# Optimization experiments

Hardware: AMD Instinct MI355X
Metric: run time of the kernel (lower is better)

Reference implementation:

```python
import jax, jax.numpy as jnp
import numpy as np

B, H, W, C = 64, 224, 224, 3
K = 16          # num_clusters
ITERS = 10      # num_iterations
N = H * W       # pixels per image


def _kmeans_single(x, key):
    # x: [N, D] pixels of one image
    # random shuffle -> first K rows as initial centroids (matches tf.random.shuffle + slice)
    perm = jax.random.permutation(key, N)
    cent0 = x[perm[:K]]  # [K, D]

    def step(cent, _):
        # pairwise squared distances: [K, N]
        d = jnp.sum(jnp.square(x[None, :, :] - cent[:, None, :]), axis=2)
        assign = jnp.argmin(d, axis=0)                      # [N] int
        onehot = jax.nn.one_hot(assign, K, dtype=x.dtype)   # [N, K]
        sums = onehot.T @ x                                 # [K, D]
        counts = jnp.sum(onehot, axis=0)[:, None]           # [K, 1]
        # mean of assigned pixels; empty cluster -> 0/0 = NaN, same as tf.reduce_mean of empty
        new_cent = sums / counts
        return new_cent, None

    cent, _ = jax.lax.scan(step, cent0, None, length=ITERS)
    return cent.reshape(K * C)  # tf.reshape(centroids, [dims*num_clusters]) on [K,D]


def setup_inputs() -> dict:
    key = jax.random.key(0)
    inputs = jax.random.uniform(key, (B, H, W, C), dtype=jnp.float32) * 255.0
    return {"inputs": inputs}


def reference(inputs):
    x = inputs.astype(jnp.float32).reshape(B, N, C)
    keys = jax.random.split(jax.random.key(42), B)
    return jax.vmap(_kmeans_single)(x, keys)  # [B, K*C]
```

## Files before the change

kernel.cpp:

```cpp
#include <hip/hip_runtime.h>
#include <stdint.h>


#define NB    64
#define NPIX  50176
#define NK    16
#define NCH   3
#define NITER 10
#define HBINS 2048
#define CANDCAP 1024
#define COLLCAP 128
#define NBLK  512
#define NGRP  8
#define GRPSZ (NBLK / NGRP)
#define CHUNK (NPIX / 8)
#define NQUADS (CHUNK / 4)

typedef unsigned long long u64;

struct KeyPair { uint32_t a, b; };

__device__ __forceinline__ uint32_t rotl32(uint32_t v, uint32_t r) {
  return (v << r) | (v >> (32u - r));
}
__device__ __forceinline__ void tf_round(uint32_t& x0, uint32_t& x1, uint32_t r) {
  x0 += x1; x1 = rotl32(x1, r); x1 ^= x0;
}

__device__ __forceinline__ KeyPair threefry(uint32_t k0, uint32_t k1,
                                            uint32_t x0, uint32_t x1) {
  const uint32_t ks2 = k0 ^ k1 ^ 0x1BD11BDAu;
  x0 += k0; x1 += k1;
  tf_round(x0, x1, 13u); tf_round(x0, x1, 15u); tf_round(x0, x1, 26u); tf_round(x0, x1, 6u);
  x0 += k1;  x1 += ks2 + 1u;
  tf_round(x0, x1, 17u); tf_round(x0, x1, 29u); tf_round(x0, x1, 16u); tf_round(x0, x1, 24u);
  x0 += ks2; x1 += k0 + 2u;
  tf_round(x0, x1, 13u); tf_round(x0, x1, 15u); tf_round(x0, x1, 26u); tf_round(x0, x1, 6u);
  x0 += k0;  x1 += k1 + 3u;
  tf_round(x0, x1, 17u); tf_round(x0, x1, 29u); tf_round(x0, x1, 16u); tf_round(x0, x1, 24u);
  x0 += k1;  x1 += ks2 + 4u;
  tf_round(x0, x1, 13u); tf_round(x0, x1, 15u); tf_round(x0, x1, 26u); tf_round(x0, x1, 6u);
  x0 += ks2; x1 += k0 + 5u;
  KeyPair r; r.a = x0; r.b = x1; return r;
}

__device__ __forceinline__ uint32_t sortkey(KeyPair S, uint32_t i) {
  KeyPair r = threefry(S.a, S.b, 0u, i);
  return r.a ^ r.b;
}

__device__ __forceinline__ void derive_keys(int b, KeyPair& S1, KeyPair& S2) {
  KeyPair root; root.a = 0u; root.b = 42u;
  KeyPair kb = threefry(root.a, root.b, 0u, (uint32_t)b);
  KeyPair K1 = threefry(kb.a, kb.b, 0u, 0u);
  S1 = threefry(kb.a, kb.b, 0u, 1u);
  S2 = threefry(K1.a, K1.b, 0u, 1u);
}

#define T2VAL 27394240u

__device__ __forceinline__ uint32_t ald_u32(const uint32_t* p) {
  return __hip_atomic_load(p, __ATOMIC_RELAXED, __HIP_MEMORY_SCOPE_AGENT);
}
__device__ __forceinline__ void ast_f64(double* p, double v) {
  __hip_atomic_store(p, v, __ATOMIC_RELAXED, __HIP_MEMORY_SCOPE_AGENT);
}
__device__ __forceinline__ double ald_f64(const double* p) {
  return __hip_atomic_load(p, __ATOMIC_RELAXED, __HIP_MEMORY_SCOPE_AGENT);
}


__device__ __forceinline__ void gbar_full(uint32_t* bar, int blk) {
  __syncthreads();
  if (threadIdx.x == 0) {
    uint32_t* grp  = bar + ((blk & (NGRP - 1)) << 4);
    uint32_t* root = bar + 128;
    uint32_t* gen  = bar + 144;
    uint32_t g = __hip_atomic_load(gen, __ATOMIC_RELAXED, __HIP_MEMORY_SCOPE_AGENT);
    __builtin_amdgcn_fence(__ATOMIC_RELEASE, "agent");
    uint32_t a = __hip_atomic_fetch_add(grp, 1u, __ATOMIC_RELAXED,
                                        __HIP_MEMORY_SCOPE_AGENT);
    if (a == (uint32_t)GRPSZ - 1u) {
      __hip_atomic_store(grp, 0u, __ATOMIC_RELAXED, __HIP_MEMORY_SCOPE_AGENT);
      uint32_t r = __hip_atomic_fetch_add(root, 1u, __ATOMIC_RELAXED,
                                          __HIP_MEMORY_SCOPE_AGENT);
      if (r == (uint32_t)NGRP - 1u) {
        __hip_atomic_store(root, 0u, __ATOMIC_RELAXED, __HIP_MEMORY_SCOPE_AGENT);
        __hip_atomic_store(gen, g + 1u, __ATOMIC_RELEASE, __HIP_MEMORY_SCOPE_AGENT);
      } else {
        while (__hip_atomic_load(gen, __ATOMIC_RELAXED,
                                 __HIP_MEMORY_SCOPE_AGENT) == g)
          __builtin_amdgcn_s_sleep(1);
      }
    } else {
      while (__hip_atomic_load(gen, __ATOMIC_RELAXED,
                               __HIP_MEMORY_SCOPE_AGENT) == g)
        __builtin_amdgcn_s_sleep(1);
    }
    __builtin_amdgcn_fence(__ATOMIC_ACQUIRE, "agent");
  }
  __syncthreads();
}

__device__ __forceinline__ void gbar_light(uint32_t* bar, int blk) {
  __syncthreads();
  if (threadIdx.x == 0) {
    uint32_t* grp  = bar + ((blk & (NGRP - 1)) << 4);
    uint32_t* root = bar + 128;
    uint32_t* gen  = bar + 144;
    uint32_t g = __hip_atomic_load(gen, __ATOMIC_RELAXED, __HIP_MEMORY_SCOPE_AGENT);
    uint32_t a = __hip_atomic_fetch_add(grp, 1u, __ATOMIC_RELEASE,
                                        __HIP_MEMORY_SCOPE_AGENT);
    if (a == (uint32_t)GRPSZ - 1u) {
      uint32_t r = __hip_atomic_fetch_add(root, 1u, __ATOMIC_RELEASE,
                                          __HIP_MEMORY_SCOPE_AGENT);
      if (r == (uint32_t)NGRP - 1u) {
        __hip_atomic_store(root, 0u, __ATOMIC_RELAXED, __HIP_MEMORY_SCOPE_AGENT);
        __hip_atomic_store(grp, 0u, __ATOMIC_RELAXED, __HIP_MEMORY_SCOPE_AGENT);
        __hip_atomic_fetch_add(gen, 1u, __ATOMIC_RELAXED, __HIP_MEMORY_SCOPE_AGENT);
      } else {
        __hip_atomic_store(grp, 0u, __ATOMIC_RELAXED, __HIP_MEMORY_SCOPE_AGENT);
        while (__hip_atomic_load(gen, __ATOMIC_RELAXED,
                                 __HIP_MEMORY_SCOPE_AGENT) == g)
          __builtin_amdgcn_s_sleep(1);
      }
    } else {
      while (__hip_atomic_load(gen, __ATOMIC_RELAXED,
                               __HIP_MEMORY_SCOPE_AGENT) == g)
        __builtin_amdgcn_s_sleep(1);
    }
  }
  __syncthreads();
}

union SMem {
  struct { uint32_t lh[HBINS]; } p1;
  struct { u64 sc[CANDCAP]; uint32_t sh[HBINS]; uint32_t S[HBINS];
           uint32_t ts[256]; uint32_t Rt[NK]; } p2;
  struct { uint32_t bs[NK]; } p3;
  struct { u64 lc[NK * COLLCAP]; int jsel[NK]; } p4;
  struct { float accf[64 * 256]; } p5;
};

__global__ __launch_bounds__(256, 2) void mega(
    const float* __restrict__ x, float* __restrict__ out,
    float* __restrict__ cent, double* __restrict__ sums,
    uint32_t* __restrict__ ncand, uint32_t* __restrict__ ncoll,
    uint32_t* __restrict__ bar, uint32_t* __restrict__ hist,
    uint32_t* __restrict__ binsel, uint32_t* __restrict__ rem,
    u64* __restrict__ cand, u64* __restrict__ coll) {
  __shared__ SMem sm;
  const int blk = (int)blockIdx.x;
  const int tid = (int)threadIdx.x;
  const int b = blk >> 3;
  const int c = blk & 7;

  KeyPair S1, S2;
  derive_keys(b, S1, S2);

  for (int i = tid; i < HBINS; i += 256) sm.p1.lh[i] = 0u;
  __syncthreads();
  {
    const int start = c * CHUNK;
    for (int i = start + tid; i < start + CHUNK; i += 256) {
      uint32_t k2 = sortkey(S2, (uint32_t)i);
      if (k2 < T2VAL) {
        uint32_t p = atomicAdd(&ncand[b], 1u);
        if (p < CANDCAP) cand[b * CANDCAP + p] = ((u64)k2 << 32) | (uint32_t)i;
      }
      uint32_t k1 = sortkey(S1, (uint32_t)i);
      atomicAdd(&sm.p1.lh[k1 >> 21], 1u);
    }
    __syncthreads();
    for (int i = tid; i < HBINS; i += 256)
      if (sm.p1.lh[i]) atomicAdd(&hist[b * HBINS + i], sm.p1.lh[i]);
  }
  gbar_full(bar, blk);

  if (blk < NB) {
    const int bb = blk;
    uint32_t nc = ald_u32(&ncand[bb]);
    const int M = nc < CANDCAP ? (int)nc : CANDCAP;
    for (int i = tid; i < M; i += 256) sm.p2.sc[i] = cand[bb * CANDCAP + i];
    for (int i = tid; i < HBINS; i += 256) sm.p2.sh[i] = hist[bb * HBINS + i];
    __syncthreads();
    for (int j = tid; j < M; j += 256) {
      u64 me = sm.p2.sc[j];
      int r = 0;
      for (int t = 0; t < M; ++t) r += (sm.p2.sc[t] < me) ? 1 : 0;
      if (r < NK) sm.p2.Rt[r] = (uint32_t)(me & 0xffffffffu);
    }
    uint32_t loc[8]; uint32_t run = 0;
    for (int j = 0; j < 8; ++j) { run += sm.p2.sh[tid * 8 + j]; loc[j] = run; }
    sm.p2.ts[tid] = run;
    __syncthreads();
    for (int off = 1; off < 256; off <<= 1) {
      uint32_t v = (tid >= off) ? sm.p2.ts[tid - off] : 0u;
      __syncthreads();
      sm.p2.ts[tid] += v;
      __syncthreads();
    }
    uint32_t excl = sm.p2.ts[tid] - run;
    for (int j = 0; j < 8; ++j) sm.p2.S[tid * 8 + j] = excl + loc[j];
    __syncthreads();
    if (tid < NK) {
      uint32_t R = sm.p2.Rt[tid];
      int lo = 0, hi = HBINS - 1;
      while (lo < hi) {
        int mid = (lo + hi) >> 1;
        if (sm.p2.S[mid] > R) hi = mid; else lo = mid + 1;
      }
      binsel[bb * NK + tid] = (uint32_t)lo;
      rem[bb * NK + tid] = R - (lo ? sm.p2.S[lo - 1] : 0u);
    }
  }
  gbar_full(bar, blk);

  {
    __shared__ uint32_t bs_s[NK];
    if (tid < NK) bs_s[tid] = binsel[b * NK + tid];
    __syncthreads();
    const int start = c * CHUNK;
    for (int i = start + tid; i < start + CHUNK; i += 256) {
      uint32_t k1 = sortkey(S1, (uint32_t)i);
      uint32_t pb = k1 >> 21;
      #pragma unroll
      for (int t = 0; t < NK; ++t) {
        if (pb == bs_s[t]) {
          uint32_t p = atomicAdd(&ncoll[b * NK + t], 1u);
          if (p < COLLCAP)
            coll[(b * NK + t) * COLLCAP + p] = ((u64)k1 << 32) | (uint32_t)i;
        }
      }
    }
  }
  gbar_full(bar, blk);

  if (blk < NB) {
    const int bb = blk;
    for (int i = tid; i < NK * COLLCAP; i += 256)
      sm.p4.lc[i] = coll[bb * NK * COLLCAP + i];
    __syncthreads();
    if (tid < NK) {
      uint32_t ncl = ncoll[bb * NK + tid];
      const int m = ncl < COLLCAP ? (int)ncl : COLLCAP;
      const uint32_t r = rem[bb * NK + tid];
      const u64* cc = &sm.p4.lc[tid * COLLCAP];
      u64 lo = 0ULL, cur = ~0ULL;
      bool first = true;
      for (uint32_t pass = 0; pass <= r; ++pass) {
        cur = ~0ULL;
        for (int i = 0; i < m; ++i) {
          u64 v = cc[i];
          if ((first || v > lo) && v < cur) cur = v;
        }
        lo = cur; first = false;
      }
      sm.p4.jsel[tid] = (int)(cur & 0xffffffffu);
    }
    __syncthreads();
    if (tid < NK * NCH) {
      int k = tid / NCH, ch = tid % NCH;
      cent[bb * NK * NCH + tid] =
          x[((size_t)bb * NPIX + (size_t)sm.p4.jsel[k]) * NCH + ch];
    }
  }
  gbar_full(bar, blk);

  const float4* px4 = (const float4*)(x + (size_t)b * NPIX * NCH + (size_t)c * (CHUNK * NCH));
  float* accf = sm.p5.accf;

  for (int it = 0; it < NITER; ++it) {
    if (tid < NK * NCH) {
      float v;
      if (it == 0) {
        v = cent[b * NK * NCH + tid];
      } else {
        const int k = tid / NCH, ch = tid - k * NCH;
        double* sb = &sums[((it - 1) % 3) * (NB * NK * 4) + b * NK * 4];
        double s = ald_f64(&sb[k * 4 + ch]);
        double n = ald_f64(&sb[k * 4 + 3]);
        v = (float)(s / n);
      }
      accf[tid] = v;
    }
    __syncthreads();
    float cr[NK * NCH];
    {
      const float4* cp = (const float4*)accf;
      #pragma unroll
      for (int i = 0; i < 12; ++i) {
        float4 t4 = cp[i];
        cr[4 * i + 0] = t4.x; cr[4 * i + 1] = t4.y;
        cr[4 * i + 2] = t4.z; cr[4 * i + 3] = t4.w;
      }
    }
    int kn = -1;
    #pragma unroll
    for (int k = NK - 1; k >= 0; --k) {
      float a = cr[3 * k], bb2 = cr[3 * k + 1], cc2 = cr[3 * k + 2];
      if (a != a || bb2 != bb2 || cc2 != cc2) kn = k;
    }
    __syncthreads();
    {
      float4 z4 = make_float4(0.f, 0.f, 0.f, 0.f);
      float4* zp = (float4*)accf;
      #pragma unroll
      for (int i = 0; i < 16; ++i) zp[tid + 256 * i] = z4;
      if (tid < NK * 4)
        ast_f64(&sums[((it + 1) % 3) * (NB * NK * 4) + b * NK * 4 + tid], 0.0);
    }
    __syncthreads();
    float* a0 = &accf[tid];
    for (int j = tid; j < NQUADS; j += 256) {
      const float4 A = px4[3 * j], Bv = px4[3 * j + 1], Cv = px4[3 * j + 2];
      const float qx[4][3] = {{A.x, A.y, A.z}, {A.w, Bv.x, Bv.y},
                              {Bv.z, Bv.w, Cv.x}, {Cv.y, Cv.z, Cv.w}};
      #pragma unroll
      for (int q = 0; q < 4; ++q) {
        const float v0 = qx[q][0], v1 = qx[q][1], v2 = qx[q][2];
        int best = 0;
        float bd = 3.402823466e38f;
        #pragma unroll
        for (int k = 0; k < NK; ++k) {
          float d0 = __fsub_rn(v0, cr[3 * k + 0]);
          float d1 = __fsub_rn(v1, cr[3 * k + 1]);
          float d2 = __fsub_rn(v2, cr[3 * k + 2]);
          float d = __fadd_rn(__fadd_rn(__fmul_rn(d0, d0), __fmul_rn(d1, d1)),
                              __fmul_rn(d2, d2));
          bool cnd = d < bd;
          bd = cnd ? d : bd;
          best = cnd ? k : best;
        }
        if (kn >= 0) best = kn;
        const int r = best << 10;
        a0[r]       += v0;
        a0[r + 256] += v1;
        a0[r + 512] += v2;
        a0[r + 768] += 1.0f;
      }
    }
    __syncthreads();
    double part = 0.0;
    {
      const int r = tid & 63, q = tid >> 6;
      const float4* rp = (const float4*)&accf[r * 256 + q * 64];
      const int s0 = r & 15;
      #pragma unroll
      for (int m = 0; m < 16; ++m) {
        float4 t4 = rp[(m + s0) & 15];
        part += (double)t4.x + (double)t4.y + (double)t4.z + (double)t4.w;
      }
    }
    __syncthreads();
    {
      double* red = (double*)accf;
      red[tid] = part;
      __syncthreads();
      if (tid < 64) {
        double tot = red[tid] + red[64 + tid] + red[128 + tid] + red[192 + tid];
        atomicAdd(&sums[(it % 3) * (NB * NK * 4) + b * NK * 4 + tid], tot);
      }
    }
    gbar_light(bar, blk);
  }

  if (c == 0 && tid < NK * NCH) {
    const int k = tid / NCH, ch = tid - k * NCH;
    double* sb = &sums[((NITER - 1) % 3) * (NB * NK * 4) + b * NK * 4];
    out[b * NK * NCH + tid] = (float)(ald_f64(&sb[k * 4 + ch]) /
                                      ald_f64(&sb[k * 4 + 3]));
  }
}

__global__ __launch_bounds__(256) void kinit_mono(const float* __restrict__ x,
                                                  float* __restrict__ cent,
                                                  float* __restrict__ sums) {
  const int b = (int)blockIdx.x;
  const int tid = (int)threadIdx.x;
  __shared__ u64 cand[CANDCAP];
  __shared__ u64 coll[NK][COLLCAP];
  __shared__ uint32_t hist[HBINS];
  __shared__ uint32_t Rtgt[NK];
  __shared__ uint32_t binsel[NK];
  __shared__ uint32_t rem[NK];
  __shared__ int jsel[NK];
  __shared__ int ncand;
  __shared__ int ncoll[NK];
  KeyPair S1, S2;
  derive_keys(b, S1, S2);
  if (tid == 0) ncand = 0;
  if (tid < NK) ncoll[tid] = 0;
  for (int i = tid; i < HBINS; i += 256) hist[i] = 0u;
  __syncthreads();
  for (int i = tid; i < NPIX; i += 256) {
    uint32_t k2 = sortkey(S2, (uint32_t)i);
    if (k2 < T2VAL) {
      int p = atomicAdd(&ncand, 1);
      if (p < CANDCAP) cand[p] = ((u64)k2 << 32) | (uint32_t)i;
    }
    uint32_t k1 = sortkey(S1, (uint32_t)i);
    atomicAdd(&hist[k1 >> 21], 1u);
  }
  __syncthreads();
  const int M = ncand < CANDCAP ? ncand : CANDCAP;
  for (int j = tid; j < M; j += 256) {
    u64 me = cand[j];
    int rank = 0;
    for (int t = 0; t < M; ++t) rank += (cand[t] < me) ? 1 : 0;
    if (rank < NK) Rtgt[rank] = (uint32_t)(me & 0xffffffffu);
  }
  __syncthreads();
  if (tid < NK) {
    uint32_t R = Rtgt[tid], cum = 0u, bin = 0u;
    for (int i = 0; i < HBINS; ++i) {
      uint32_t h = hist[i];
      if (R < cum + h) { bin = (uint32_t)i; break; }
      cum += h;
    }
    binsel[tid] = bin;
    rem[tid] = R - cum;
  }
  __syncthreads();
  for (int i = tid; i < NPIX; i += 256) {
    uint32_t k1 = sortkey(S1, (uint32_t)i);
    uint32_t pb = k1 >> 21;
    #pragma unroll
    for (int t = 0; t < NK; ++t) {
      if (pb == binsel[t]) {
        int p = atomicAdd(&ncoll[t], 1);
        if (p < COLLCAP) coll[t][p] = ((u64)k1 << 32) | (uint32_t)i;
      }
    }
  }
  __syncthreads();
  if (tid < NK) {
    int m = ncoll[tid] < COLLCAP ? ncoll[tid] : COLLCAP;
    uint32_t r = rem[tid];
    u64 lo = 0ULL, cur = ~0ULL;
    bool first = true;
    for (uint32_t pass = 0; pass <= r; ++pass) {
      cur = ~0ULL;
      for (int t = 0; t < m; ++t) {
        u64 v = coll[tid][t];
        if ((first || v > lo) && v < cur) cur = v;
      }
      lo = cur; first = false;
    }
    jsel[tid] = (int)(cur & 0xffffffffu);
  }
  __syncthreads();
  if (tid < NK * NCH) {
    int k = tid / NCH, c = tid % NCH;
    cent[(b * NK + k) * NCH + c] = x[((size_t)b * NPIX + (size_t)jsel[k]) * NCH + c];
  }
  if (tid < NK * 4) sums[b * NK * 4 + tid] = 0.0f;
}

__global__ __launch_bounds__(256) void kassign(const float* __restrict__ x,
                                               const float* __restrict__ cent,
                                               float* __restrict__ sums) {
  const int b = (int)blockIdx.y;
  const int tid = (int)threadIdx.x;
  __shared__ float cs[NK * NCH];
  __shared__ float acc[4][NK * 4];
  __shared__ int knan_s;
  if (tid < NK * NCH) cs[tid] = cent[b * NK * NCH + tid];
  acc[tid >> 6][tid & 63] = 0.0f;
  __syncthreads();
  if (tid == 0) {
    int kn = -1;
    for (int k = 0; k < NK; ++k) {
      float a = cs[3 * k], bb = cs[3 * k + 1], cc = cs[3 * k + 2];
      if (a != a || bb != bb || cc != cc) { kn = k; break; }
    }
    knan_s = kn;
  }
  __syncthreads();
  float cr[NK * NCH];
  #pragma unroll
  for (int i = 0; i < NK * NCH; ++i) cr[i] = cs[i];
  const float* xb = x + (size_t)b * NPIX * NCH;
  const float4* p = (const float4*)(xb + (size_t)blockIdx.x * 3072);
  const float4 A = p[3 * tid], Bv = p[3 * tid + 1], Cv = p[3 * tid + 2];
  const float px[4][3] = {{A.x, A.y, A.z}, {A.w, Bv.x, Bv.y},
                          {Bv.z, Bv.w, Cv.x}, {Cv.y, Cv.z, Cv.w}};
  float* a0 = acc[tid >> 6];
  const int kn = knan_s;
  #pragma unroll
  for (int q = 0; q < 4; ++q) {
    const float v0 = px[q][0], v1 = px[q][1], v2 = px[q][2];
    int best = 0;
    float bd = 3.402823466e38f;
    #pragma unroll
    for (int k = 0; k < NK; ++k) {
      float d0 = __fsub_rn(v0, cr[3 * k + 0]);
      float d1 = __fsub_rn(v1, cr[3 * k + 1]);
      float d2 = __fsub_rn(v2, cr[3 * k + 2]);
      float d = __fadd_rn(__fadd_rn(__fmul_rn(d0, d0), __fmul_rn(d1, d1)),
                          __fmul_rn(d2, d2));
      bool cnd = d < bd;
      bd = cnd ? d : bd;
      best = cnd ? k : best;
    }
    if (kn >= 0) best = kn;
    atomicAdd(&a0[best * 4 + 0], v0);
    atomicAdd(&a0[best * 4 + 1], v1);
    atomicAdd(&a0[best * 4 + 2], v2);
    atomicAdd(&a0[best * 4 + 3], 1.0f);
  }
  __syncthreads();
  if (tid < NK * 4) {
    float v = acc[0][tid] + acc[1][tid] + acc[2][tid] + acc[3][tid];
    atomicAdd(&sums[b * NK * 4 + tid], v);
  }
}

__global__ __launch_bounds__(64) void kupdate(float* __restrict__ cent,
                                              float* __restrict__ sums,
                                              float* __restrict__ out) {
  const int b = (int)blockIdx.x;
  const int t = (int)threadIdx.x;
  float v = 0.0f;
  if (t < NK * NCH) {
    const int k = t / NCH, c = t % NCH;
    v = sums[b * NK * 4 + k * 4 + c] / sums[b * NK * 4 + k * 4 + 3];
  }
  __syncthreads();
  if (t < NK * NCH) {
    cent[b * NK * NCH + t] = v;
    out[b * NK * NCH + t] = v;
  }
  sums[b * NK * 4 + t] = 0.0f;
}

extern "C" void kernel_launch(void* const* d_in, const int* in_sizes, int n_in,
                              void* d_out, int out_size, void* d_ws, size_t ws_size,
                              hipStream_t stream) {
  (void)in_sizes; (void)n_in; (void)out_size;
  const float* x = (const float*)d_in[0];
  float* out = (float*)d_out;
  char* ws = (char*)d_ws;

  float*    cent   = (float*)(ws + 0);
  double*   sums   = (double*)(ws + 12288);
  uint32_t* ncand  = (uint32_t*)(ws + 110592);
  uint32_t* ncoll  = (uint32_t*)(ws + 110848);
  uint32_t* bar    = (uint32_t*)(ws + 114944);
  uint32_t* hist   = (uint32_t*)(ws + 115968);
  uint32_t* binsel = (uint32_t*)(ws + 640256);
  uint32_t* rem    = (uint32_t*)(ws + 644352);
  u64*      cand   = (u64*)(ws + 648448);
  u64*      coll   = (u64*)(ws + 1172736);
  const size_t REQ = 2221312;

  if (ws_size >= REQ) {
    hipMemsetAsync(ws + 110592, 0, 529664, stream);
    mega<<<NBLK, 256, 0, stream>>>(x, out, cent, sums, ncand, ncoll, bar,
                                   hist, binsel, rem, cand, coll);
  } else {
    float* centf = (float*)ws;
    float* sumsf = centf + NB * NK * NCH;
    kinit_mono<<<NB, 256, 0, stream>>>(x, centf, sumsf);
    for (int it = 0; it < NITER; ++it) {
      kassign<<<dim3(49, NB), 256, 0, stream>>>(x, centf, sumsf);
      kupdate<<<NB, 64, 0, stream>>>(centf, sumsf, out);
    }
  }
}
```

Measured before the change: 549.1 us.

## Replace grid-wide barriers with per-image 8-block barriers

Swaps the hierarchical grid barrier across all 512 blocks for a barrier scoped to the 8 blocks that work on the same image, using a monotonically increasing per-image counter with a phase target. The per-image serial stages now run in the block with c==0 of each image instead of in the first 64 blocks. This cuts barrier latency and lets images progress independently, at the cost of relying on the counter never being reset and on all 8 blocks of an image being co-resident. Spin sleep is also lengthened.

```diff
diff --git a/kernel.cpp b/kernel.cpp
--- a/kernel.cpp
+++ b/kernel.cpp
@@ -11,8 +11,6 @@
 #define CANDCAP 1024
 #define COLLCAP 128
 #define NBLK  512
-#define NGRP  8
-#define GRPSZ (NBLK / NGRP)
 #define CHUNK (NPIX / 8)
 #define NQUADS (CHUNK / 4)
 
@@ -70,65 +68,32 @@
 }
 
 
-__device__ __forceinline__ void gbar_full(uint32_t* bar, int blk) {
+__device__ __forceinline__ void bbar_full(uint32_t* bar, int b, int& ph) {
   __syncthreads();
   if (threadIdx.x == 0) {
-    uint32_t* grp  = bar + ((blk & (NGRP - 1)) << 4);
-    uint32_t* root = bar + 128;
-    uint32_t* gen  = bar + 144;
-    uint32_t g = __hip_atomic_load(gen, __ATOMIC_RELAXED, __HIP_MEMORY_SCOPE_AGENT);
+    uint32_t* slot = bar + (b << 2);
+    ph += 1;
+    const uint32_t tgt = (uint32_t)(ph << 3);
     __builtin_amdgcn_fence(__ATOMIC_RELEASE, "agent");
-    uint32_t a = __hip_atomic_fetch_add(grp, 1u, __ATOMIC_RELAXED,
-                                        __HIP_MEMORY_SCOPE_AGENT);
-    if (a == (uint32_t)GRPSZ - 1u) {
-      __hip_atomic_store(grp, 0u, __ATOMIC_RELAXED, __HIP_MEMORY_SCOPE_AGENT);
-      uint32_t r = __hip_atomic_fetch_add(root, 1u, __ATOMIC_RELAXED,
-                                          __HIP_MEMORY_SCOPE_AGENT);
-      if (r == (uint32_t)NGRP - 1u) {
-        __hip_atomic_store(root, 0u, __ATOMIC_RELAXED, __HIP_MEMORY_SCOPE_AGENT);
-        __hip_atomic_store(gen, g + 1u, __ATOMIC_RELEASE, __HIP_MEMORY_SCOPE_AGENT);
-      } else {
-        while (__hip_atomic_load(gen, __ATOMIC_RELAXED,
-                                 __HIP_MEMORY_SCOPE_AGENT) == g)
-          __builtin_amdgcn_s_sleep(1);
-      }
-    } else {
-      while (__hip_atomic_load(gen, __ATOMIC_RELAXED,
-                               __HIP_MEMORY_SCOPE_AGENT) == g)
-        __builtin_amdgcn_s_sleep(1);
-    }
+    __hip_atomic_fetch_add(slot, 1u, __ATOMIC_RELEASE, __HIP_MEMORY_SCOPE_AGENT);
+    while (__hip_atomic_load(slot, __ATOMIC_RELAXED,
+                             __HIP_MEMORY_SCOPE_AGENT) < tgt)
+      __builtin_amdgcn_s_sleep(4);
     __builtin_amdgcn_fence(__ATOMIC_ACQUIRE, "agent");
   }
   __syncthreads();
 }
 
-__device__ __forceinline__ void gbar_light(uint32_t* bar, int blk) {
+__device__ __forceinline__ void bbar_light(uint32_t* bar, int b, int& ph) {
   __syncthreads();
   if (threadIdx.x == 0) {
-    uint32_t* grp  = bar + ((blk & (NGRP - 1)) << 4);
-    uint32_t* root = bar + 128;
-    uint32_t* gen  = bar + 144;
-    uint32_t g = __hip_atomic_load(gen, __ATOMIC_RELAXED, __HIP_MEMORY_SCOPE_AGENT);
-    uint32_t a = __hip_atomic_fetch_add(grp, 1u, __ATOMIC_RELEASE,
-                                        __HIP_MEMORY_SCOPE_AGENT);
-    if (a == (uint32_t)GRPSZ - 1u) {
-      uint32_t r = __hip_atomic_fetch_add(root, 1u, __ATOMIC_RELEASE,
-                                          __HIP_MEMORY_SCOPE_AGENT);
-      if (r == (uint32_t)NGRP - 1u) {
-        __hip_atomic_store(root, 0u, __ATOMIC_RELAXED, __HIP_MEMORY_SCOPE_AGENT);
-        __hip_atomic_store(grp, 0u, __ATOMIC_RELAXED, __HIP_MEMORY_SCOPE_AGENT);
-        __hip_atomic_fetch_add(gen, 1u, __ATOMIC_RELAXED, __HIP_MEMORY_SCOPE_AGENT);
-      } else {
-        __hip_atomic_store(grp, 0u, __ATOMIC_RELAXED, __HIP_MEMORY_SCOPE_AGENT);
-        while (__hip_atomic_load(gen, __ATOMIC_RELAXED,
-                                 __HIP_MEMORY_SCOPE_AGENT) == g)
-          __builtin_amdgcn_s_sleep(1);
-      }
-    } else {
-      while (__hip_atomic_load(gen, __ATOMIC_RELAXED,
-                               __HIP_MEMORY_SCOPE_AGENT) == g)
-        __builtin_amdgcn_s_sleep(1);
-    }
+    uint32_t* slot = bar + (b << 2);
+    ph += 1;
+    const uint32_t tgt = (uint32_t)(ph << 3);
+    __hip_atomic_fetch_add(slot, 1u, __ATOMIC_RELEASE, __HIP_MEMORY_SCOPE_AGENT);
+    while (__hip_atomic_load(slot, __ATOMIC_RELAXED,
+                             __HIP_MEMORY_SCOPE_AGENT) < tgt)
+      __builtin_amdgcn_s_sleep(4);
   }
   __syncthreads();
 }
@@ -154,6 +119,7 @@
   const int tid = (int)threadIdx.x;
   const int b = blk >> 3;
   const int c = blk & 7;
+  int ph = 0;
 
   KeyPair S1, S2;
   derive_keys(b, S1, S2);
@@ -175,10 +141,10 @@
     for (int i = tid; i < HBINS; i += 256)
       if (sm.p1.lh[i]) atomicAdd(&hist[b * HBINS + i], sm.p1.lh[i]);
   }
-  gbar_full(bar, blk);
-
-  if (blk < NB) {
-    const int bb = blk;
+  bbar_full(bar, b, ph);
+
+  if (c == 0) {
+    const int bb = b;
     uint32_t nc = ald_u32(&ncand[bb]);
     const int M = nc < CANDCAP ? (int)nc : CANDCAP;
     for (int i = tid; i < M; i += 256) sm.p2.sc[i] = cand[bb * CANDCAP + i];
@@ -214,7 +180,7 @@
       rem[bb * NK + tid] = R - (lo ? sm.p2.S[lo - 1] : 0u);
     }
   }
-  gbar_full(bar, blk);
+  bbar_full(bar, b, ph);
 
   {
     __shared__ uint32_t bs_s[NK];
@@ -234,10 +200,10 @@
       }
     }
   }
-  gbar_full(bar, blk);
-
-  if (blk < NB) {
-    const int bb = blk;
+  bbar_full(bar, b, ph);
+
+  if (c == 0) {
+    const int bb = b;
     for (int i = tid; i < NK * COLLCAP; i += 256)
       sm.p4.lc[i] = coll[bb * NK * COLLCAP + i];
     __syncthreads();
@@ -265,7 +231,7 @@
           x[((size_t)bb * NPIX + (size_t)sm.p4.jsel[k]) * NCH + ch];
     }
   }
-  gbar_full(bar, blk);
+  bbar_full(bar, b, ph);
 
   const float4* px4 = (const float4*)(x + (size_t)b * NPIX * NCH + (size_t)c * (CHUNK * NCH));
   float* accf = sm.p5.accf;
@@ -362,7 +328,7 @@
         atomicAdd(&sums[(it % 3) * (NB * NK * 4) + b * NK * 4 + tid], tot);
       }
     }
-    gbar_light(bar, blk);
+    bbar_light(bar, b, ph);
   }
 
   if (c == 0 && tid < NK * NCH) {
```

Measured after the change: 496.1 us. 9.7% less time.
